# Performance work log

Hardware: AMD Instinct MI355X
Metric: run time of the kernel (lower is better)

Reference implementation:

```python
import jax, jax.numpy as jnp
import numpy as np

NUM_TOKENS = 131072
INPUT_DIM = 1024
NUM_EXPERTS = 8
TOP_K = 2


def setup_inputs() -> dict:
    key = jax.random.key(0)
    kx, kw, kb = jax.random.split(key, 3)
    x = jax.random.normal(kx, (NUM_TOKENS, INPUT_DIM), dtype=jnp.float32)
    # nn.Linear(input_dim, num_experts): W [E, D], b [E]
    lim = 1.0 / np.sqrt(INPUT_DIM)
    W = jax.random.uniform(kw, (NUM_EXPERTS, INPUT_DIM), dtype=jnp.float32, minval=-lim, maxval=lim)
    b = jax.random.uniform(kb, (NUM_EXPERTS,), dtype=jnp.float32, minval=-lim, maxval=lim)
    return {"x": x, "W": W, "b": b}


def reference(x, W, b):
    # gating_scores = gate(x): [N, E]
    logits = jnp.einsum('nd,ed->ne', x, W) + b
    probs = jax.nn.softmax(logits, axis=1)
    # torch.topk returns (values, indices); module returns (indices, values)
    top_k_values, top_k_indices = jax.lax.top_k(probs, TOP_K)
    return (top_k_indices, top_k_values)
```

## Files before the change

kernel.cpp:

```cpp
#include <hip/hip_runtime.h>
#include <math.h>


#define NUM_TOKENS 131072
#define DIM        1024
#define NE         8
#define TPB        256
#define DC         64
#define ROWSTRIDE  68

__global__ __launch_bounds__(TPB)
void topk_gating_kernel(const float* __restrict__ x,
                        const float* __restrict__ W,
                        const float* __restrict__ b,
                        float* __restrict__ out)
{
    __shared__ float lds[TPB * ROWSTRIDE];
    const int t    = threadIdx.x;
    const int tok0 = blockIdx.x * TPB;

    float acc[NE];
#pragma unroll
    for (int e = 0; e < NE; ++e) acc[e] = 0.f;

    const float4* x4   = (const float4*)x;
    const float4* W4   = (const float4*)W;
    float4*       lds4 = (float4*)lds;

    for (int c = 0; c < DIM / DC; ++c) {
        __syncthreads();
#pragma unroll
        for (int l = 0; l < 16; ++l) {
            int flat = l * TPB + t;
            int r    = flat >> 4;
            int c4   = flat & 15;
            float4 v = x4[(tok0 + r) * (DIM / 4) + c * (DC / 4) + c4];
            lds4[r * (ROWSTRIDE / 4) + c4] = v;
        }
        __syncthreads();
#pragma unroll 4
        for (int j = 0; j < DC / 4; ++j) {
            float4 xv = lds4[t * (ROWSTRIDE / 4) + j];
            int d = c * (DC / 4) + j;
#pragma unroll
            for (int e = 0; e < NE; ++e) {
                float4 w = W4[e * (DIM / 4) + d];
                acc[e] = fmaf(xv.x, w.x, acc[e]);
                acc[e] = fmaf(xv.y, w.y, acc[e]);
                acc[e] = fmaf(xv.z, w.z, acc[e]);
                acc[e] = fmaf(xv.w, w.w, acc[e]);
            }
        }
    }

    float logit[NE];
#pragma unroll
    for (int e = 0; e < NE; ++e) logit[e] = acc[e] + b[e];

    float v1 = -INFINITY, v2 = -INFINITY;
    int   i1 = 0,         i2 = 0;
#pragma unroll
    for (int e = 0; e < NE; ++e) {
        float v = logit[e];
        if (v > v1)      { v2 = v1; i2 = i1; v1 = v; i1 = e; }
        else if (v > v2) { v2 = v;  i2 = e; }
    }

    float sum = 0.f;
#pragma unroll
    for (int e = 0; e < NE; ++e) sum += __expf(logit[e] - v1);
    float inv = 1.0f / sum;
    float p1  = inv;
    float p2  = __expf(v2 - v1) * inv;

    int n = tok0 + t;
    float2* outi = (float2*)out;
    float2* outv = (float2*)(out + 2 * (size_t)NUM_TOKENS);
    outi[n] = make_float2((float)i1, (float)i2);
    outv[n] = make_float2(p1, p2);
}

extern "C" void kernel_launch(void* const* d_in, const int* in_sizes, int n_in,
                              void* d_out, int out_size, void* d_ws, size_t ws_size,
                              hipStream_t stream) {
    const float* x = (const float*)d_in[0];
    const float* W = (const float*)d_in[1];
    const float* b = (const float*)d_in[2];
    float* out = (float*)d_out;

    dim3 grid(NUM_TOKENS / TPB);
    dim3 block(TPB);
    topk_gating_kernel<<<grid, block, 0, stream>>>(x, W, b, out);
}
```

Baseline: 779.0 us.

## Use per-wave LDS tiles with register prefetch pipeline instead of block barriers

Result: slower. 914.3 us (+17.4%).

```diff
diff --git a/kernel.cpp b/kernel.cpp
--- a/kernel.cpp
+++ b/kernel.cpp
@@ -6,8 +6,10 @@
 #define DIM        1024
 #define NE         8
 #define TPB        256
-#define DC         64
-#define ROWSTRIDE  68
+#define DC         32
+#define NCH        (DIM / DC)
+#define PD         4
+#define RS4        9
 
 __global__ __launch_bounds__(TPB)
 void topk_gating_kernel(const float* __restrict__ x,
@@ -15,40 +17,60 @@
                         const float* __restrict__ b,
                         float* __restrict__ out)
 {
-    __shared__ float lds[TPB * ROWSTRIDE];
+    __shared__ float4 lds4[4][64 * RS4];
     const int t    = threadIdx.x;
+    const int lane = t & 63;
+    const int w    = t >> 6;
     const int tok0 = blockIdx.x * TPB;
+
+    const float4* x4 = (const float4*)x;
+    const float4* W4 = (const float4*)W;
+    float4* lw = lds4[w];
+
+    const int rb  = lane >> 3;
+    const int c4  = lane & 7;
+    const int row0 = tok0 + w * 64;
 
     float acc[NE];
 #pragma unroll
     for (int e = 0; e < NE; ++e) acc[e] = 0.f;
 
-    const float4* x4   = (const float4*)x;
-    const float4* W4   = (const float4*)W;
-    float4*       lds4 = (float4*)lds;
+    float4 pre[PD][8];
 
-    for (int c = 0; c < DIM / DC; ++c) {
-        __syncthreads();
 #pragma unroll
-        for (int l = 0; l < 16; ++l) {
-            int flat = l * TPB + t;
-            int r    = flat >> 4;
-            int c4   = flat & 15;
-            float4 v = x4[(tok0 + r) * (DIM / 4) + c * (DC / 4) + c4];
-            lds4[r * (ROWSTRIDE / 4) + c4] = v;
-        }
-        __syncthreads();
-#pragma unroll 4
-        for (int j = 0; j < DC / 4; ++j) {
-            float4 xv = lds4[t * (ROWSTRIDE / 4) + j];
-            int d = c * (DC / 4) + j;
+    for (int p = 0; p < PD; ++p)
 #pragma unroll
-            for (int e = 0; e < NE; ++e) {
-                float4 w = W4[e * (DIM / 4) + d];
-                acc[e] = fmaf(xv.x, w.x, acc[e]);
-                acc[e] = fmaf(xv.y, w.y, acc[e]);
-                acc[e] = fmaf(xv.z, w.z, acc[e]);
-                acc[e] = fmaf(xv.w, w.w, acc[e]);
+        for (int i = 0; i < 8; ++i)
+            pre[p][i] = x4[(row0 + i * 8 + rb) * (DIM / 4) + p * (DC / 4) + c4];
+
+    for (int cc = 0; cc < NCH; cc += PD) {
+#pragma unroll
+        for (int p = 0; p < PD; ++p) {
+            const int ch = cc + p;
+
+#pragma unroll
+            for (int i = 0; i < 8; ++i)
+                lw[(i * 8 + rb) * RS4 + c4] = pre[p][i];
+
+            if (ch + PD < NCH) {
+#pragma unroll
+                for (int i = 0; i < 8; ++i)
+                    pre[p][i] = x4[(row0 + i * 8 + rb) * (DIM / 4)
+                                   + (ch + PD) * (DC / 4) + c4];
+            }
+
+#pragma unroll
+            for (int j = 0; j < DC / 4; ++j) {
+                float4 xv = lw[lane * RS4 + j];
+                int d = ch * (DC / 4) + j;
+#pragma unroll
+                for (int e = 0; e < NE; ++e) {
+                    float4 wv = W4[e * (DIM / 4) + d];
+                    acc[e] = fmaf(xv.x, wv.x, acc[e]);
+                    acc[e] = fmaf(xv.y, wv.y, acc[e]);
+                    acc[e] = fmaf(xv.z, wv.z, acc[e]);
+                    acc[e] = fmaf(xv.w, wv.w, acc[e]);
+                }
             }
         }
     }
```
